# Optimization experiments

Measured on AMD Instinct MI355X. Metric: run time of the kernel, lower is better.

The kernel has to match this reference:

```python
import jax, jax.numpy as jnp
import numpy as np

B, T, D_MODEL, H, D = 2, 2048, 1024, 16, 64
EPS = 1e-5


def _layernorm(x, g, b):
    m = jnp.mean(x, axis=-1, keepdims=True)
    v = jnp.var(x, axis=-1, keepdims=True)
    return (x - m) * jax.lax.rsqrt(v + EPS) * g + b


def setup_inputs() -> dict:
    key = jax.random.key(0)
    ks = jax.random.split(key, 5)
    qab = H * D
    x = jax.random.normal(ks[0], (B, T, D_MODEL), dtype=jnp.float32)
    sc = 1.0 / np.sqrt(D_MODEL)
    Wq = jax.random.normal(ks[1], (D_MODEL, qab), dtype=jnp.float32) * sc
    Wa = jax.random.normal(ks[2], (D_MODEL, qab), dtype=jnp.float32) * sc
    Wb = jax.random.normal(ks[3], (D_MODEL, qab), dtype=jnp.float32) * sc
    Wo = jax.random.normal(ks[4], (qab, D_MODEL), dtype=jnp.float32) * (1.0 / np.sqrt(qab))
    g = jnp.ones((D,), dtype=jnp.float32)
    z = jnp.zeros((D,), dtype=jnp.float32)
    return {"x": x, "Wq": Wq, "Wa": Wa, "Wb": Wb, "Wo": Wo,
            "q_gamma": g, "q_beta": z, "a_gamma": g, "a_beta": z,
            "b_gamma": g, "b_beta": z}


def reference(x, Wq, Wa, Wb, Wo, q_gamma, q_beta, a_gamma, a_beta, b_gamma, b_beta):
    def split_heads(y):  # (B,T,H*D) -> (B,H,T,D)
        Bx, Tx, _ = y.shape
        return y.reshape(Bx, Tx, H, D).transpose(0, 2, 1, 3)

    q = _layernorm(split_heads(x @ Wq), q_gamma, q_beta)
    a = _layernorm(split_heads(x @ Wa), a_gamma, a_beta)
    b = _layernorm(split_heads(x @ Wb), b_gamma, b_beta)

    # strict-exclusive cumsum of a along time
    a_excl = jnp.cumsum(a, axis=-2) - a
    # o_t = q_t . sum_{j<=t} a_excl_j (x) b_j  ==  causal (q a_excl^T) b
    scores = jnp.einsum('bhtd,bhsd->bhts', q, a_excl)  # (B,H,T,T)
    causal = jnp.tril(jnp.ones((T, T), dtype=scores.dtype))  # j <= t
    o = jnp.einsum('bhts,bhse->bhte', scores * causal, b)  # (B,H,T,D)

    o = o.transpose(0, 2, 1, 3).reshape(B, T, H * D)  # merge heads
    return o @ Wo
```

## Files before the change

### kernel.cpp

```cpp
#include <hip/hip_runtime.h>
#include <hip/hip_bf16.h>

#define T_LEN  2048
#define NHEAD  16
#define HDIM   64
#define DMODEL 1024
#define BATCH  2
#define MROWS  4096
#define L_CHK  64
#define N_CHK  (T_LEN / L_CHK)
#define BH     (BATCH * NHEAD)

typedef __attribute__((ext_vector_type(8))) short short8;
typedef __attribute__((ext_vector_type(4))) float f32x4;
typedef __attribute__((ext_vector_type(4))) unsigned short ushort4v;

#define GLDS(GP, LP) __builtin_amdgcn_global_load_lds( \
    (__attribute__((address_space(1))) void*)(void*)(GP), \
    (__attribute__((address_space(3))) void*)(LP), 16, 0, 0)

__device__ __forceinline__ unsigned short f2bf(float f) {
  union { float f; unsigned int u; } v; v.f = f;
  unsigned int r = v.u + 0x7FFFu + ((v.u >> 16) & 1u);
  return (unsigned short)(r >> 16);
}
__device__ __forceinline__ float bf2f(short s) {
  union { unsigned int u; float f; } v;
  v.u = ((unsigned int)(unsigned short)s) << 16;
  return v.f;
}

__global__ __launch_bounds__(256) void ha_conv(
    const float* __restrict__ Wq, const float* __restrict__ Wa,
    const float* __restrict__ Wb, const float* __restrict__ Wo,
    const float* __restrict__ X,
    short* __restrict__ wqabT, short* __restrict__ woT,
    short* __restrict__ Xb) {
  const int z = blockIdx.z;
  const int tid = threadIdx.x;
  if (z == 4) {
    const int bidl = blockIdx.y * 16 + blockIdx.x;
    #pragma unroll
    for (int p = 0; p < 8; ++p) {
      const size_t idx = (size_t)bidl * 16384 + (size_t)p * 2048 + tid * 8;
      float4 v0 = *(const float4*)(X + idx);
      float4 v1 = *(const float4*)(X + idx + 4);
      short8 o;
      o[0] = (short)f2bf(v0.x); o[1] = (short)f2bf(v0.y);
      o[2] = (short)f2bf(v0.z); o[3] = (short)f2bf(v0.w);
      o[4] = (short)f2bf(v1.x); o[5] = (short)f2bf(v1.y);
      o[6] = (short)f2bf(v1.z); o[7] = (short)f2bf(v1.w);
      *(short8*)(Xb + idx) = o;
    }
    return;
  }
  __shared__ float tile[64][65];
  const float* W = (z == 0) ? Wq : (z == 1) ? Wa : (z == 2) ? Wb : Wo;
  short* WT = (z < 3) ? wqabT + (size_t)z * 1024 * DMODEL : woT;
  const int k0 = blockIdx.y * 64, n0 = blockIdx.x * 64;
  #pragma unroll
  for (int p = 0; p < 4; ++p) {
    const int r  = p * 16 + (tid >> 4);
    const int c4 = (tid & 15) * 4;
    float4 v = *(const float4*)(W + (size_t)(k0 + r) * DMODEL + n0 + c4);
    tile[r][c4 + 0] = v.x; tile[r][c4 + 1] = v.y;
    tile[r][c4 + 2] = v.z; tile[r][c4 + 3] = v.w;
  }
  __syncthreads();
  #pragma unroll
  for (int p = 0; p < 4; ++p) {
    const int n = p * 16 + (tid >> 4);
    const int c = (tid & 15) * 4;
    ushort4v o = { f2bf(tile[c + 0][n]), f2bf(tile[c + 1][n]),
                   f2bf(tile[c + 2][n]), f2bf(tile[c + 3][n]) };
    *(ushort4v*)(WT + (size_t)(n0 + n) * DMODEL + k0 + c) = o;
  }
}

__global__ __launch_bounds__(256) void ha_gemm_qab(
    const short* __restrict__ Ab, const short* __restrict__ Bt,
    short* __restrict__ q, short* __restrict__ a, short* __restrict__ bOut,
    const float* __restrict__ qg, const float* __restrict__ qbet,
    const float* __restrict__ ag, const float* __restrict__ abet,
    const float* __restrict__ bg, const float* __restrict__ bbet) {
  __shared__ short As[128 * 32] __attribute__((aligned(16)));
  __shared__ short Bs[128 * 32] __attribute__((aligned(16)));
  const int tid = threadIdx.x;
  const int wave = tid >> 6, lane = tid & 63;
  const int m0  = blockIdx.y * 128;
  const int n0g = blockIdx.x * 128;
  short* Cbuf; const float* gamma; const float* beta;
  if (n0g < 1024)      { Cbuf = q;    gamma = qg; beta = qbet; }
  else if (n0g < 2048) { Cbuf = a;    gamma = ag; beta = abet; }
  else                 { Cbuf = bOut; gamma = bg; beta = bbet; }
  const int n0 = n0g & 1023;

  const int srow = wave * 32 + (lane >> 2);
  const int scol = (lane & 3) * 8;
  const short* agp = Ab + (size_t)(m0 + srow) * DMODEL + scol;
  const short* bgp = Bt + (size_t)(n0g + srow) * DMODEL + scol;
  short* alp = As + wave * 32 * 32;
  short* blp = Bs + wave * 32 * 32;

  f32x4 acc[4][4] = {};
  const int lm = lane & 15, kh = lane >> 4;
  const int wm = (wave >> 1) * 64, wn = (wave & 1) * 64;

  float gl[4], bl[4];
  #pragma unroll
  for (int j = 0; j < 4; ++j) {
    gl[j] = gamma[j * 16 + lm];
    bl[j] = beta[j * 16 + lm];
  }

  for (int k0 = 0; k0 < DMODEL; k0 += 32) {
    GLDS(agp,               alp);
    GLDS(agp + 16 * DMODEL, alp + 16 * 32);
    GLDS(bgp,               blp);
    GLDS(bgp + 16 * DMODEL, blp + 16 * 32);
    agp += 32; bgp += 32;
    __syncthreads();
    short8 af[4], bf[4];
    #pragma unroll
    for (int i = 0; i < 4; ++i) {
      af[i] = *(const short8*)&As[(wm + i * 16 + lm) * 32 + kh * 8];
      bf[i] = *(const short8*)&Bs[(wn + i * 16 + lm) * 32 + kh * 8];
    }
    #pragma unroll
    for (int i = 0; i < 4; ++i)
      #pragma unroll
      for (int j = 0; j < 4; ++j)
        acc[i][j] = __builtin_amdgcn_mfma_f32_16x16x32_bf16(
            af[i], bf[j], acc[i][j], 0, 0, 0);
    __syncthreads();
  }

  #pragma unroll
  for (int i = 0; i < 4; ++i) {
    float s1[4] = {0.f, 0.f, 0.f, 0.f};
    float s2[4] = {0.f, 0.f, 0.f, 0.f};
    #pragma unroll
    for (int j = 0; j < 4; ++j)
      #pragma unroll
      for (int r = 0; r < 4; ++r) {
        const float v = acc[i][j][r];
        s1[r] += v; s2[r] += v * v;
      }
    #pragma unroll
    for (int m = 1; m <= 8; m <<= 1)
      #pragma unroll
      for (int r = 0; r < 4; ++r) {
        s1[r] += __shfl_xor(s1[r], m);
        s2[r] += __shfl_xor(s2[r], m);
      }
    #pragma unroll
    for (int r = 0; r < 4; ++r) {
      const float mean = s1[r] * 0.015625f;
      const float var  = s2[r] * 0.015625f - mean * mean;
      const float rs   = rsqrtf(var + 1e-5f);
      short* cp = Cbuf + (size_t)(m0 + wm + i * 16 + kh * 4 + r) * DMODEL +
                  n0 + wn + lm;
      #pragma unroll
      for (int j = 0; j < 4; ++j)
        cp[j * 16] = (short)f2bf((acc[i][j][r] - mean) * rs * gl[j] + bl[j]);
    }
  }
}

__global__ __launch_bounds__(256) void ha_gemm_out(
    const short* __restrict__ Ab, const short* __restrict__ Bt,
    float* __restrict__ C) {
  __shared__ short As[128 * 32] __attribute__((aligned(16)));
  __shared__ short Bs[64 * 32] __attribute__((aligned(16)));
  const int tid = threadIdx.x;
  const int wave = tid >> 6, lane = tid & 63;
  const int m0 = blockIdx.y * 128;
  const int n0 = blockIdx.x * 64;

  const int arow = wave * 32 + (lane >> 2);
  const int brow = wave * 16 + (lane >> 2);
  const int scol = (lane & 3) * 8;
  const short* agp = Ab + (size_t)(m0 + arow) * DMODEL + scol;
  const short* bgp = Bt + (size_t)(n0 + brow) * DMODEL + scol;
  short* alp = As + wave * 32 * 32;
  short* blp = Bs + wave * 16 * 32;

  f32x4 acc[4][2] = {};
  const int lm = lane & 15, kh = lane >> 4;
  const int wm = (wave >> 1) * 64, wn = (wave & 1) * 32;

  for (int k0 = 0; k0 < DMODEL; k0 += 32) {
    GLDS(agp,               alp);
    GLDS(agp + 16 * DMODEL, alp + 16 * 32);
    GLDS(bgp,               blp);
    agp += 32; bgp += 32;
    __syncthreads();
    short8 af[4], bf2[2];
    #pragma unroll
    for (int i = 0; i < 4; ++i)
      af[i] = *(const short8*)&As[(wm + i * 16 + lm) * 32 + kh * 8];
    #pragma unroll
    for (int j = 0; j < 2; ++j)
      bf2[j] = *(const short8*)&Bs[(wn + j * 16 + lm) * 32 + kh * 8];
    #pragma unroll
    for (int i = 0; i < 4; ++i)
      #pragma unroll
      for (int j = 0; j < 2; ++j)
        acc[i][j] = __builtin_amdgcn_mfma_f32_16x16x32_bf16(
            af[i], bf2[j], acc[i][j], 0, 0, 0);
    __syncthreads();
  }
  #pragma unroll
  for (int i = 0; i < 4; ++i)
    #pragma unroll
    for (int j = 0; j < 2; ++j) {
      float* cp = C + (size_t)(m0 + wm + i * 16 + kh * 4) * DMODEL +
                  n0 + wn + j * 16 + lm;
      #pragma unroll
      for (int r = 0; r < 4; ++r) cp[(size_t)r * DMODEL] = acc[i][j][r];
    }
}

__global__ __launch_bounds__(256) void ha_scan1(
    const short* __restrict__ An, const short* __restrict__ Bn,
    float* __restrict__ M, float* __restrict__ Asums, float* __restrict__ Bsums) {
  __shared__ float Al[64][68];
  __shared__ float Bl[64][68];
  __shared__ float sega[4][64];
  __shared__ float segb[4][64];
  const int bid = blockIdx.x;
  const int c   = bid & (N_CHK - 1);
  const int bh  = bid >> 5;
  const int b = bh >> 4, h = bh & 15;
  const int tid = threadIdx.x;
  const size_t rowbase = ((size_t)b * T_LEN + (size_t)c * L_CHK) * DMODEL + h * HDIM;

  #pragma unroll
  for (int i = 0; i < 2; ++i) {
    const int idx = tid + 256 * i;
    const int s = idx >> 3, c8 = (idx & 7) * 8;
    short8 a8 = *(const short8*)(An + rowbase + (size_t)s * DMODEL + c8);
    short8 b8 = *(const short8*)(Bn + rowbase + (size_t)s * DMODEL + c8);
    #pragma unroll
    for (int k = 0; k < 8; ++k) {
      Al[s][c8 + k] = bf2f(a8[k]);
      Bl[s][c8 + k] = bf2f(b8[k]);
    }
  }
  __syncthreads();

  const int d = tid & 63, seg = tid >> 6;
  {
    float run = 0.f, runb = 0.f;
    for (int s = seg * 16; s < seg * 16 + 16; ++s) {
      const float va = Al[s][d];
      Al[s][d] = run;
      run  += va;
      runb += Bl[s][d];
    }
    sega[seg][d] = run;
    segb[seg][d] = runb;
  }
  __syncthreads();
  {
    float off = 0.f;
    for (int qq = 0; qq < seg; ++qq) off += sega[qq][d];
    for (int s = seg * 16; s < seg * 16 + 16; ++s) Al[s][d] += off;
    if (seg == 0) {
      Asums[((size_t)bh * N_CHK + c) * 64 + d] =
          sega[0][d] + sega[1][d] + sega[2][d] + sega[3][d];
      Bsums[((size_t)bh * N_CHK + c) * 64 + d] =
          segb[0][d] + segb[1][d] + segb[2][d] + segb[3][d];
    }
  }
  __syncthreads();

  const int e0 = (tid >> 4) * 4, d0 = (tid & 15) * 4;
  float acc[4][4];
  #pragma unroll
  for (int i = 0; i < 4; ++i)
    #pragma unroll
    for (int j = 0; j < 4; ++j) acc[i][j] = 0.f;
  #pragma unroll 8
  for (int s = 0; s < 64; ++s) {
    const float4 bv = *(const float4*)&Bl[s][e0];
    const float4 av = *(const float4*)&Al[s][d0];
    const float bb_[4] = {bv.x, bv.y, bv.z, bv.w};
    const float aa_[4] = {av.x, av.y, av.z, av.w};
    #pragma unroll
    for (int i = 0; i < 4; ++i)
      #pragma unroll
      for (int j = 0; j < 4; ++j) acc[i][j] = fmaf(bb_[i], aa_[j], acc[i][j]);
  }
  float* Mp = M + ((size_t)bh * N_CHK + c) * 4096;
  #pragma unroll
  for (int i = 0; i < 4; ++i)
    *(float4*)(Mp + (e0 + i) * 64 + d0) =
        make_float4(acc[i][0], acc[i][1], acc[i][2], acc[i][3]);
}

__global__ __launch_bounds__(256) void ha_s2p(
    float* __restrict__ M, const float* __restrict__ Asums,
    const float* __restrict__ Bsums, float* __restrict__ Aoff) {
  __shared__ float ao[N_CHK][64];
  const int part = blockIdx.x & 7;
  const int bh   = blockIdx.x >> 3;
  const int tid  = threadIdx.x;
  for (int i = tid; i < N_CHK * 64; i += 256)
    ao[i >> 6][i & 63] = Asums[(size_t)bh * N_CHK * 64 + i];
  __syncthreads();
  if (tid < 64) {
    float run = 0.f;
    for (int c = 0; c < N_CHK; ++c) {
      const float v = ao[c][tid];
      ao[c][tid] = run;
      run += v;
    }
  }
  __syncthreads();
  if (part == 0)
    for (int i = tid; i < N_CHK * 64; i += 256)
      Aoff[(size_t)bh * N_CHK * 64 + i] = ao[i >> 6][i & 63];

  const int e = part * 8 + (tid >> 5);
  const int d = (tid & 31) * 2;
  float2 S = make_float2(0.f, 0.f);
  for (int c = 0; c < N_CHK; ++c) {
    const float bs = Bsums[((size_t)bh * N_CHK + c) * 64 + e];
    const float aox = ao[c][d], aoy = ao[c][d + 1];
    float* Mp = M + ((size_t)bh * N_CHK + c) * 4096 + e * 64 + d;
    const float2 m = *(const float2*)Mp;
    *(float2*)Mp = S;
    S.x += fmaf(bs, aox, m.x);
    S.y += fmaf(bs, aoy, m.y);
  }
}

__global__ __launch_bounds__(256) void ha_scan3(
    const short* __restrict__ Qn, const short* __restrict__ An,
    const short* __restrict__ Bn, const float* __restrict__ Soff,
    const float* __restrict__ Aoff, short* __restrict__ Ob) {
  __shared__ float Qt[64][68];
  __shared__ float Gt[64][68];
  __shared__ float Bl[64][68];
  __shared__ float Pt[64][68];
  const int bid = blockIdx.x;
  const int c   = bid & (N_CHK - 1);
  const int bh  = bid >> 5;
  const int b = bh >> 4, h = bh & 15;
  const int tid = threadIdx.x;
  const size_t rowbase = ((size_t)b * T_LEN + (size_t)c * L_CHK) * DMODEL + h * HDIM;

  #pragma unroll
  for (int i = 0; i < 2; ++i) {
    const int idx = tid + 256 * i;
    const int t = idx >> 3, c8 = (idx & 7) * 8;
    short8 q8 = *(const short8*)(Qn + rowbase + (size_t)t * DMODEL + c8);
    short8 a8 = *(const short8*)(An + rowbase + (size_t)t * DMODEL + c8);
    short8 b8 = *(const short8*)(Bn + rowbase + (size_t)t * DMODEL + c8);
    #pragma unroll
    for (int k = 0; k < 8; ++k) {
      Qt[c8 + k][t] = bf2f(q8[k]);
      Gt[c8 + k][t] = bf2f(a8[k]);
      Bl[t][c8 + k] = bf2f(b8[k]);
    }
  }
  __syncthreads();

  if (tid < 64) {
    float run = Aoff[((size_t)bh * N_CHK + c) * 64 + tid];
    for (int s = 0; s < 64; ++s) {
      const float v = Gt[tid][s];
      Gt[tid][s] = run;
      run += v;
    }
  }
  __syncthreads();

  const int tt = tid >> 4, ss = tid & 15;
  const int t0 = tt * 4, s0 = ss * 4;
  {
    float p[4][4];
    #pragma unroll
    for (int i = 0; i < 4; ++i)
      #pragma unroll
      for (int j = 0; j < 4; ++j) p[i][j] = 0.f;
    #pragma unroll 8
    for (int k = 0; k < 64; ++k) {
      const float4 qv = *(const float4*)&Qt[k][t0];
      const float4 gv = *(const float4*)&Gt[k][s0];
      const float qq[4] = {qv.x, qv.y, qv.z, qv.w};
      const float gg[4] = {gv.x, gv.y, gv.z, gv.w};
      #pragma unroll
      for (int i = 0; i < 4; ++i)
        #pragma unroll
        for (int j = 0; j < 4; ++j) p[i][j] = fmaf(qq[i], gg[j], p[i][j]);
    }
    #pragma unroll
    for (int i = 0; i < 4; ++i)
      #pragma unroll
      for (int j = 0; j < 4; ++j)
        Pt[s0 + j][t0 + i] = (s0 + j <= t0 + i) ? p[i][j] : 0.f;
  }
  __syncthreads();

  const float* Sg = Soff + ((size_t)bh * N_CHK + c) * 4096;
  #pragma unroll
  for (int i = 0; i < 4; ++i) {
    const int idx = tid + 256 * i;
    const int e = idx >> 4, d4 = idx & 15;
    float4 s4 = *(const float4*)(Sg + (size_t)e * 64 + d4 * 4);
    Gt[d4 * 4 + 0][e] = s4.x; Gt[d4 * 4 + 1][e] = s4.y;
    Gt[d4 * 4 + 2][e] = s4.z; Gt[d4 * 4 + 3][e] = s4.w;
  }
  __syncthreads();

  const int e0 = s0;
  float o[4][4];
  #pragma unroll
  for (int i = 0; i < 4; ++i)
    #pragma unroll
    for (int j = 0; j < 4; ++j) o[i][j] = 0.f;
  #pragma unroll 8
  for (int s = 0; s < 64; ++s) {
    const float4 pv = *(const float4*)&Pt[s][t0];
    const float4 bv = *(const float4*)&Bl[s][e0];
    const float pp[4] = {pv.x, pv.y, pv.z, pv.w};
    const float bb_[4] = {bv.x, bv.y, bv.z, bv.w};
    #pragma unroll
    for (int i = 0; i < 4; ++i)
      #pragma unroll
      for (int j = 0; j < 4; ++j) o[i][j] = fmaf(pp[i], bb_[j], o[i][j]);
  }
  #pragma unroll 8
  for (int dd = 0; dd < 64; ++dd) {
    const float4 qv = *(const float4*)&Qt[dd][t0];
    const float4 sv = *(const float4*)&Gt[dd][e0];
    const float qq[4] = {qv.x, qv.y, qv.z, qv.w};
    const float sS[4] = {sv.x, sv.y, sv.z, sv.w};
    #pragma unroll
    for (int i = 0; i < 4; ++i)
      #pragma unroll
      for (int j = 0; j < 4; ++j) o[i][j] = fmaf(qq[i], sS[j], o[i][j]);
  }
  #pragma unroll
  for (int i = 0; i < 4; ++i) {
    ushort4v o4 = { f2bf(o[i][0]), f2bf(o[i][1]), f2bf(o[i][2]), f2bf(o[i][3]) };
    *(ushort4v*)(Ob + rowbase + (size_t)(t0 + i) * DMODEL + e0) = o4;
  }
}

extern "C" void kernel_launch(void* const* d_in, const int* in_sizes, int n_in,
                              void* d_out, int out_size, void* d_ws,
                              size_t ws_size, hipStream_t stream) {
  const float* x  = (const float*)d_in[0];
  const float* Wq = (const float*)d_in[1];
  const float* Wa = (const float*)d_in[2];
  const float* Wb = (const float*)d_in[3];
  const float* Wo = (const float*)d_in[4];
  const float* qg = (const float*)d_in[5];
  const float* qb = (const float*)d_in[6];
  const float* ag = (const float*)d_in[7];
  const float* ab = (const float*)d_in[8];
  const float* bg = (const float*)d_in[9];
  const float* bb = (const float*)d_in[10];
  float* out = (float*)d_out;

  char* ws = (char*)d_ws;
  short* qn  = (short*)(ws);
  short* an  = (short*)(ws + ((size_t)8  << 20));
  short* bn  = (short*)(ws + ((size_t)16 << 20));
  short* xb  = (short*)(ws + ((size_t)24 << 20));
  short* obb = xb;
  short* wqabT = (short*)(ws + ((size_t)32 << 20));
  short* woT   = (short*)(ws + ((size_t)38 << 20));
  float* asums = (float*)(ws + ((size_t)40 << 20));
  float* bsums = asums + (size_t)BH * N_CHK * 64;
  float* aoff  = bsums + (size_t)BH * N_CHK * 64;
  float* Mbuf  = out;

  ha_conv<<<dim3(16, 16, 5), 256, 0, stream>>>(Wq, Wa, Wb, Wo, x,
                                               wqabT, woT, xb);

  ha_gemm_qab<<<dim3(24, 32), 256, 0, stream>>>(xb, wqabT, qn, an, bn,
                                                qg, qb, ag, ab, bg, bb);

  ha_scan1<<<BH * N_CHK, 256, 0, stream>>>(an, bn, Mbuf, asums, bsums);
  ha_s2p<<<BH * 8, 256, 0, stream>>>(Mbuf, asums, bsums, aoff);
  ha_scan3<<<BH * N_CHK, 256, 0, stream>>>(qn, an, bn, Mbuf, aoff, obb);

  ha_gemm_out<<<dim3(16, 32), 256, 0, stream>>>(obb, woT, out);
}
```

Measured before the change: 204.1 us.

## Move chunked scan matmuls to bf16 MFMA and store chunk states as bf16

```diff
diff --git a/kernel.cpp b/kernel.cpp
--- a/kernel.cpp
+++ b/kernel.cpp
@@ -10,6 +10,7 @@
 #define L_CHK  64
 #define N_CHK  (T_LEN / L_CHK)
 #define BH     (BATCH * NHEAD)
+#define LSTR   72
 
 typedef __attribute__((ext_vector_type(8))) short short8;
 typedef __attribute__((ext_vector_type(4))) float f32x4;
@@ -224,8 +225,8 @@
 __global__ __launch_bounds__(256) void ha_scan1(
     const short* __restrict__ An, const short* __restrict__ Bn,
     float* __restrict__ M, float* __restrict__ Asums, float* __restrict__ Bsums) {
-  __shared__ float Al[64][68];
-  __shared__ float Bl[64][68];
+  __shared__ short Btl[64 * LSTR] __attribute__((aligned(16)));
+  __shared__ short Ltl[64 * LSTR] __attribute__((aligned(16)));
   __shared__ float sega[4][64];
   __shared__ float segb[4][64];
   const int bid = blockIdx.x;
@@ -234,74 +235,77 @@
   const int b = bh >> 4, h = bh & 15;
   const int tid = threadIdx.x;
   const size_t rowbase = ((size_t)b * T_LEN + (size_t)c * L_CHK) * DMODEL + h * HDIM;
+  const size_t vec = ((size_t)bh * N_CHK + c) * 64;
 
   #pragma unroll
   for (int i = 0; i < 2; ++i) {
     const int idx = tid + 256 * i;
     const int s = idx >> 3, c8 = (idx & 7) * 8;
-    short8 a8 = *(const short8*)(An + rowbase + (size_t)s * DMODEL + c8);
     short8 b8 = *(const short8*)(Bn + rowbase + (size_t)s * DMODEL + c8);
     #pragma unroll
-    for (int k = 0; k < 8; ++k) {
-      Al[s][c8 + k] = bf2f(a8[k]);
-      Bl[s][c8 + k] = bf2f(b8[k]);
-    }
-  }
-  __syncthreads();
+    for (int k = 0; k < 8; ++k) Btl[(c8 + k) * LSTR + s] = b8[k];
+  }
 
   const int d = tid & 63, seg = tid >> 6;
   {
-    float run = 0.f, runb = 0.f;
+    float run = 0.f;
     for (int s = seg * 16; s < seg * 16 + 16; ++s) {
-      const float va = Al[s][d];
-      Al[s][d] = run;
-      run  += va;
-      runb += Bl[s][d];
+      const float v = bf2f(An[rowbase + (size_t)s * DMODEL + d]);
+      Ltl[d * LSTR + s] = (short)f2bf(run);
+      run += v;
     }
     sega[seg][d] = run;
-    segb[seg][d] = runb;
   }
   __syncthreads();
   {
     float off = 0.f;
     for (int qq = 0; qq < seg; ++qq) off += sega[qq][d];
-    for (int s = seg * 16; s < seg * 16 + 16; ++s) Al[s][d] += off;
-    if (seg == 0) {
-      Asums[((size_t)bh * N_CHK + c) * 64 + d] =
-          sega[0][d] + sega[1][d] + sega[2][d] + sega[3][d];
-      Bsums[((size_t)bh * N_CHK + c) * 64 + d] =
-          segb[0][d] + segb[1][d] + segb[2][d] + segb[3][d];
-    }
-  }
-  __syncthreads();
-
-  const int e0 = (tid >> 4) * 4, d0 = (tid & 15) * 4;
-  float acc[4][4];
-  #pragma unroll
-  for (int i = 0; i < 4; ++i)
-    #pragma unroll
-    for (int j = 0; j < 4; ++j) acc[i][j] = 0.f;
-  #pragma unroll 8
-  for (int s = 0; s < 64; ++s) {
-    const float4 bv = *(const float4*)&Bl[s][e0];
-    const float4 av = *(const float4*)&Al[s][d0];
-    const float bb_[4] = {bv.x, bv.y, bv.z, bv.w};
-    const float aa_[4] = {av.x, av.y, av.z, av.w};
-    #pragma unroll
-    for (int i = 0; i < 4; ++i)
-      #pragma unroll
-      for (int j = 0; j < 4; ++j) acc[i][j] = fmaf(bb_[i], aa_[j], acc[i][j]);
-  }
-  float* Mp = M + ((size_t)bh * N_CHK + c) * 4096;
-  #pragma unroll
-  for (int i = 0; i < 4; ++i)
-    *(float4*)(Mp + (e0 + i) * 64 + d0) =
-        make_float4(acc[i][0], acc[i][1], acc[i][2], acc[i][3]);
+    #pragma unroll
+    for (int g = 0; g < 2; ++g) {
+      short8 v = *(short8*)&Ltl[d * LSTR + seg * 16 + g * 8];
+      #pragma unroll
+      for (int k = 0; k < 8; ++k) v[k] = (short)f2bf(bf2f(v[k]) + off);
+      *(short8*)&Ltl[d * LSTR + seg * 16 + g * 8] = v;
+    }
+    if (seg == 3) Asums[vec + d] = off + sega[3][d];
+    float sb = 0.f;
+    #pragma unroll
+    for (int g = 0; g < 2; ++g) {
+      short8 v = *(const short8*)&Btl[d * LSTR + seg * 16 + g * 8];
+      #pragma unroll
+      for (int k = 0; k < 8; ++k) sb += bf2f(v[k]);
+    }
+    segb[seg][d] = sb;
+  }
+  __syncthreads();
+  if (tid < 64)
+    Bsums[vec + tid] = segb[0][tid] + segb[1][tid] + segb[2][tid] + segb[3][tid];
+
+  const int wave = tid >> 6, lane = tid & 63;
+  const int lm = lane & 15, quad = lane >> 4;
+  const int estrip = wave * 16;
+  f32x4 acc[4] = {};
+  #pragma unroll
+  for (int kk = 0; kk < 2; ++kk) {
+    short8 afr = *(const short8*)&Btl[(estrip + lm) * LSTR + kk * 32 + quad * 8];
+    #pragma unroll
+    for (int j = 0; j < 4; ++j) {
+      short8 bfr = *(const short8*)&Ltl[(j * 16 + lm) * LSTR + kk * 32 + quad * 8];
+      acc[j] = __builtin_amdgcn_mfma_f32_16x16x32_bf16(afr, bfr, acc[j], 0, 0, 0);
+    }
+  }
+  float* Mp = M + vec * 64;
+  #pragma unroll
+  for (int j = 0; j < 4; ++j)
+    #pragma unroll
+    for (int r = 0; r < 4; ++r)
+      Mp[(estrip + quad * 4 + r) * 64 + j * 16 + lm] = acc[j][r];
 }
 
 __global__ __launch_bounds__(256) void ha_s2p(
-    float* __restrict__ M, const float* __restrict__ Asums,
-    const float* __restrict__ Bsums, float* __restrict__ Aoff) {
+    const float* __restrict__ M, const float* __restrict__ Asums,
+    const float* __restrict__ Bsums, float* __restrict__ Aoff,
+    short* __restrict__ Soffb) {
   __shared__ float ao[N_CHK][64];
   const int part = blockIdx.x & 7;
   const int bh   = blockIdx.x >> 3;
@@ -325,128 +329,126 @@
   const int e = part * 8 + (tid >> 5);
   const int d = (tid & 31) * 2;
   float2 S = make_float2(0.f, 0.f);
+  const float* Mp = M + (size_t)bh * N_CHK * 4096 + e * 64 + d;
+  const float* Bp = Bsums + (size_t)bh * N_CHK * 64 + e;
+  short* Sp = Soffb + (size_t)bh * N_CHK * 4096 + e * 64 + d;
+  float2 m = *(const float2*)Mp;
+  float bs = *Bp;
   for (int c = 0; c < N_CHK; ++c) {
-    const float bs = Bsums[((size_t)bh * N_CHK + c) * 64 + e];
-    const float aox = ao[c][d], aoy = ao[c][d + 1];
-    float* Mp = M + ((size_t)bh * N_CHK + c) * 4096 + e * 64 + d;
-    const float2 m = *(const float2*)Mp;
-    *(float2*)Mp = S;
-    S.x += fmaf(bs, aox, m.x);
-    S.y += fmaf(bs, aoy, m.y);
+    const int cn = (c + 1 < N_CHK) ? c + 1 : c;
+    const float2 mn = *(const float2*)(Mp + (size_t)cn * 4096);
+    const float bsn = Bp[(size_t)cn * 64];
+    const unsigned pk = (unsigned)f2bf(S.x) | ((unsigned)f2bf(S.y) << 16);
+    *(unsigned*)(Sp + (size_t)c * 4096) = pk;
+    S.x += fmaf(bs, ao[c][d], m.x);
+    S.y += fmaf(bs, ao[c][d + 1], m.y);
+    m = mn; bs = bsn;
   }
 }
 
 __global__ __launch_bounds__(256) void ha_scan3(
     const short* __restrict__ Qn, const short* __restrict__ An,
-    const short* __restrict__ Bn, const float* __restrict__ Soff,
+    const short* __restrict__ Bn, const short* __restrict__ Soffb,
     const float* __restrict__ Aoff, short* __restrict__ Ob) {
-  __shared__ float Qt[64][68];
-  __shared__ float Gt[64][68];
-  __shared__ float Bl[64][68];
-  __shared__ float Pt[64][68];
+  __shared__ short Qs [64 * LSTR] __attribute__((aligned(16)));
+  __shared__ short Gs [64 * LSTR] __attribute__((aligned(16)));
+  __shared__ short Btl[64 * LSTR] __attribute__((aligned(16)));
+  __shared__ short Ssl[64 * LSTR] __attribute__((aligned(16)));
+  __shared__ short Ptl[64 * LSTR] __attribute__((aligned(16)));
+  __shared__ float sega[4][64];
   const int bid = blockIdx.x;
   const int c   = bid & (N_CHK - 1);
   const int bh  = bid >> 5;
   const int b = bh >> 4, h = bh & 15;
   const int tid = threadIdx.x;
   const size_t rowbase = ((size_t)b * T_LEN + (size_t)c * L_CHK) * DMODEL + h * HDIM;
+  const size_t vec = ((size_t)bh * N_CHK + c) * 64;
 
   #pragma unroll
   for (int i = 0; i < 2; ++i) {
     const int idx = tid + 256 * i;
-    const int t = idx >> 3, c8 = (idx & 7) * 8;
-    short8 q8 = *(const short8*)(Qn + rowbase + (size_t)t * DMODEL + c8);
-    short8 a8 = *(const short8*)(An + rowbase + (size_t)t * DMODEL + c8);
-    short8 b8 = *(const short8*)(Bn + rowbase + (size_t)t * DMODEL + c8);
-    #pragma unroll
-    for (int k = 0; k < 8; ++k) {
-      Qt[c8 + k][t] = bf2f(q8[k]);
-      Gt[c8 + k][t] = bf2f(a8[k]);
-      Bl[t][c8 + k] = bf2f(b8[k]);
-    }
-  }
-  __syncthreads();
-
-  if (tid < 64) {
-    float run = Aoff[((size_t)bh * N_CHK + c) * 64 + tid];
-    for (int s = 0; s < 64; ++s) {
-      const float v = Gt[tid][s];
-      Gt[tid][s] = run;
+    const int r = idx >> 3, c8 = (idx & 7) * 8;
+    short8 q8 = *(const short8*)(Qn + rowbase + (size_t)r * DMODEL + c8);
+    *(short8*)&Qs[r * LSTR + c8] = q8;
+    short8 s8 = *(const short8*)(Soffb + vec * 64 + (size_t)r * 64 + c8);
+    *(short8*)&Ssl[r * LSTR + c8] = s8;
+    short8 b8 = *(const short8*)(Bn + rowbase + (size_t)r * DMODEL + c8);
+    #pragma unroll
+    for (int k = 0; k < 8; ++k) Btl[(c8 + k) * LSTR + r] = b8[k];
+  }
+
+  const int d = tid & 63, seg = tid >> 6;
+  {
+    float run = 0.f;
+    for (int s = seg * 16; s < seg * 16 + 16; ++s) {
+      const float v = bf2f(An[rowbase + (size_t)s * DMODEL + d]);
+      Gs[s * LSTR + d] = (short)f2bf(run);
       run += v;
     }
-  }
-  __syncthreads();
-
-  const int tt = tid >> 4, ss = tid & 15;
-  const int t0 = tt * 4, s0 = ss * 4;
-  {
-    float p[4][4];
-    #pragma unroll
-    for (int i = 0; i < 4; ++i)
-      #pragma unroll
-      for (int j = 0; j < 4; ++j) p[i][j] = 0.f;
-    #pragma unroll 8
-    for (int k = 0; k < 64; ++k) {
-      const float4 qv = *(const float4*)&Qt[k][t0];
-      const float4 gv = *(const float4*)&Gt[k][s0];
-      const float qq[4] = {qv.x, qv.y, qv.z, qv.w};
-      const float gg[4] = {gv.x, gv.y, gv.z, gv.w};
-      #pragma unroll
-      for (int i = 0; i < 4; ++i)
-        #pragma unroll
-        for (int j = 0; j < 4; ++j) p[i][j] = fmaf(qq[i], gg[j], p[i][j]);
-    }
-    #pragma unroll
-    for (int i = 0; i < 4; ++i)
-      #pragma unroll
-      for (int j = 0; j < 4; ++j)
-        Pt[s0 + j][t0 + i] = (s0 + j <= t0 + i) ? p[i][j] : 0.f;
-  }
-  __syncthreads();
-
-  const float* Sg = Soff + ((size_t)bh * N_CHK + c) * 4096;
-  #pragma unroll
-  for (int i = 0; i < 4; ++i) {
-    const int idx = tid + 256 * i;
-    const int e = idx >> 4, d4 = idx & 15;
-    float4 s4 = *(const float4*)(Sg + (size_t)e * 64 + d4 * 4);
-    Gt[d4 * 4 + 0][e] = s4.x; Gt[d4 * 4 + 1][e] = s4.y;
-    Gt[d4 * 4 + 2][e] = s4.z; Gt[d4 * 4 + 3][e] = s4.w;
-  }
-  __syncthreads();
-
-  const int e0 = s0;
-  float o[4][4];
-  #pragma unroll
-  for (int i = 0; i < 4; ++i)
-    #pragma unroll
-    for (int j = 0; j < 4; ++j) o[i][j] = 0.f;
-  #pragma unroll 8
-  for (int s = 0; s < 64; ++s) {
-    const float4 pv = *(const float4*)&Pt[s][t0];
-    const float4 bv = *(const float4*)&Bl[s][e0];
-    const float pp[4] = {pv.x, pv.y, pv.z, pv.w};
-    const float bb_[4] = {bv.x, bv.y, bv.z, bv.w};
-    #pragma unroll
-    for (int i = 0; i < 4; ++i)
-      #pragma unroll
-      for (int j = 0; j < 4; ++j) o[i][j] = fmaf(pp[i], bb_[j], o[i][j]);
-  }
-  #pragma unroll 8
-  for (int dd = 0; dd < 64; ++dd) {
-    const float4 qv = *(const float4*)&Qt[dd][t0];
-    const float4 sv = *(const float4*)&Gt[dd][e0];
-    const float qq[4] = {qv.x, qv.y, qv.z, qv.w};
-    const float sS[4] = {sv.x, sv.y, sv.z, sv.w};
-    #pragma unroll
-    for (int i = 0; i < 4; ++i)
-      #pragma unroll
-      for (int j = 0; j < 4; ++j) o[i][j] = fmaf(qq[i], sS[j], o[i][j]);
-  }
-  #pragma unroll
-  for (int i = 0; i < 4; ++i) {
-    ushort4v o4 = { f2bf(o[i][0]), f2bf(o[i][1]), f2bf(o[i][2]), f2bf(o[i][3]) };
-    *(ushort4v*)(Ob + rowbase + (size_t)(t0 + i) * DMODEL + e0) = o4;
+    sega[seg][d] = run;
+  }
+  __syncthreads();
+  {
+    float off = Aoff[vec + d];
+    for (int qq = 0; qq < seg; ++qq) off += sega[qq][d];
+    for (int s = seg * 16; s < seg * 16 + 16; ++s)
+      Gs[s * LSTR + d] = (short)f2bf(bf2f(Gs[s * LSTR + d]) + off);
+  }
+  __syncthreads();
+
+  const int wave = tid >> 6, lane = tid & 63;
+  const int lm = lane & 15, quad = lane >> 4;
+  const int tstrip = wave * 16;
+  {
+    f32x4 p[4] = {};
+    #pragma unroll
+    for (int kk = 0; kk < 2; ++kk) {
+      short8 qf = *(const short8*)&Qs[(tstrip + lm) * LSTR + kk * 32 + quad * 8];
+      #pragma unroll
+      for (int j = 0; j < 4; ++j) {
+        short8 gf = *(const short8*)&Gs[(j * 16 + lm) * LSTR + kk * 32 + quad * 8];
+        p[j] = __builtin_amdgcn_mfma_f32_16x16x32_bf16(qf, gf, p[j], 0, 0, 0);
+      }
+    }
+    #pragma unroll
+    for (int j = 0; j < 4; ++j)
+      #pragma unroll
+      for (int r = 0; r < 4; ++r) {
+        const int t = tstrip + quad * 4 + r;
+        const int s = j * 16 + lm;
+        Ptl[t * LSTR + s] = (s <= t) ? (short)f2bf(p[j][r]) : (short)0;
+      }
+  }
+  __syncthreads();
+
+  {
+    f32x4 o[4] = {};
+    #pragma unroll
+    for (int kk = 0; kk < 2; ++kk) {
+      short8 pf = *(const short8*)&Ptl[(tstrip + lm) * LSTR + kk * 32 + quad * 8];
+      #pragma unroll
+      for (int j = 0; j < 4; ++j) {
+        short8 bfr = *(const short8*)&Btl[(j * 16 + lm) * LSTR + kk * 32 + quad * 8];
+        o[j] = __builtin_amdgcn_mfma_f32_16x16x32_bf16(pf, bfr, o[j], 0, 0, 0);
+      }
+    }
+    #pragma unroll
+    for (int kk = 0; kk < 2; ++kk) {
+      short8 qf = *(const short8*)&Qs[(tstrip + lm) * LSTR + kk * 32 + quad * 8];
+      #pragma unroll
+      for (int j = 0; j < 4; ++j) {
+        short8 sf = *(const short8*)&Ssl[(j * 16 + lm) * LSTR + kk * 32 + quad * 8];
+        o[j] = __builtin_amdgcn_mfma_f32_16x16x32_bf16(qf, sf, o[j], 0, 0, 0);
+      }
+    }
+    #pragma unroll
+    for (int j = 0; j < 4; ++j)
+      #pragma unroll
+      for (int r = 0; r < 4; ++r) {
+        const int t = tstrip + quad * 4 + r;
+        const int e = j * 16 + lm;
+        Ob[rowbase + (size_t)t * DMODEL + e] = (short)f2bf(o[j][r]);
+      }
   }
 }
 
@@ -477,6 +479,7 @@
   float* asums = (float*)(ws + ((size_t)40 << 20));
   float* bsums = asums + (size_t)BH * N_CHK * 64;
   float* aoff  = bsums + (size_t)BH * N_CHK * 64;
+  short* soffb = (short*)(ws + ((size_t)42 << 20));
   float* Mbuf  = out;
 
   ha_conv<<<dim3(16, 16, 5), 256, 0, stream>>>(Wq, Wa, Wb, Wo, x,
@@ -486,8 +489,8 @@
                                                 qg, qb, ag, ab, bg, bb);
 
   ha_scan1<<<BH * N_CHK, 256, 0, stream>>>(an, bn, Mbuf, asums, bsums);
-  ha_s2p<<<BH * 8, 256, 0, stream>>>(Mbuf, asums, bsums, aoff);
-  ha_scan3<<<BH * N_CHK, 256, 0, stream>>>(qn, an, bn, Mbuf, aoff, obb);
+  ha_s2p<<<BH * 8, 256, 0, stream>>>(Mbuf, asums, bsums, aoff, soffb);
+  ha_scan3<<<BH * N_CHK, 256, 0, stream>>>(qn, an, bn, soffb, aoff, obb);
 
   ha_gemm_out<<<dim3(16, 32), 256, 0, stream>>>(obb, woT, out);
 }
```

Result: faster. 182.3 us (-10.7%).
